# Performance work log

Hardware: AMD Instinct MI355X
Metric: run time of the kernel (lower is better)

The kernel has to match this reference:

```python
import jax, jax.numpy as jnp
import numpy as np

BS, T, LAB, DEMO, HID, F = 1024, 128, 64, 16, 32, 4


def setup_inputs() -> dict:
    key = jax.random.key(0)
    ks = jax.random.split(key, 12)
    s = 0.1
    return {
        "x": jax.random.normal(ks[0], (BS, T, LAB), dtype=jnp.float32),
        "static": jax.random.normal(ks[1], (BS, DEMO), dtype=jnp.float32),
        "demo_W": jax.random.normal(ks[2], (HID, DEMO), dtype=jnp.float32) * s,
        "demo_b": jax.random.normal(ks[3], (HID,), dtype=jnp.float32) * s,
        "lab_W": jax.random.normal(ks[4], (LAB, LAB), dtype=jnp.float32) * s,
        "lab_b": jax.random.normal(ks[5], (LAB,), dtype=jnp.float32) * s,
        # per-lab GRU weights stacked over lab_dim; input size is 1 so W_ih is [LAB, 3F]
        "Wih": jax.random.normal(ks[6], (LAB, 3 * F), dtype=jnp.float32) * 0.5,
        "bih": jax.random.normal(ks[7], (LAB, 3 * F), dtype=jnp.float32) * 0.5,
        "Whh": jax.random.normal(ks[8], (LAB, 3 * F, F), dtype=jnp.float32) * 0.5,
        "bhh": jax.random.normal(ks[9], (LAB, 3 * F), dtype=jnp.float32) * 0.5,
        "out_W": jax.random.normal(ks[10], (HID, LAB * F + HID), dtype=jnp.float32) * s,
        "out_b": jax.random.normal(ks[11], (HID,), dtype=jnp.float32) * s,
    }


def reference(x, static, demo_W, demo_b, lab_W, lab_b, Wih, bih, Whh, bhh, out_W, out_b):
    bs, t, lab = x.shape
    f = Whh.shape[-1]
    demo = static @ demo_W.T + demo_b                     # [bs, HID]
    xp = x @ lab_W.T + lab_b                              # [bs, T, LAB]

    def step(h, x_t):
        # h: [bs, LAB, F], x_t: [bs, LAB] (scalar input per lab-GRU)
        gi = x_t[:, :, None] * Wih[None] + bih[None]      # [bs, LAB, 3F]
        gh = jnp.einsum('blf,lgf->blg', h, Whh) + bhh[None]
        r = jax.nn.sigmoid(gi[..., :f] + gh[..., :f])
        z = jax.nn.sigmoid(gi[..., f:2 * f] + gh[..., f:2 * f])
        n = jnp.tanh(gi[..., 2 * f:] + r * gh[..., 2 * f:])
        h_new = (1.0 - z) * n + z * h
        return h_new, None

    h0 = jnp.zeros((bs, lab, f), dtype=x.dtype)
    h_last, _ = jax.lax.scan(step, h0, jnp.swapaxes(xp, 0, 1))  # only final step is used
    feat = h_last.reshape(bs, lab * f)                     # [bs, LAB*F]
    cat = jnp.concatenate([demo, feat], axis=-1)
    return cat @ out_W.T + out_b                           # [bs, HID]
```

## Files before the change

kernel.cpp:

```cpp
#include <hip/hip_runtime.h>
#include <cstddef>

#define BSZ   1024
#define TT    128
#define LAB   64
#define DEMO  16
#define HID   32
#define FF    4

__device__ __forceinline__ float sig_s(float p) {
    return __builtin_amdgcn_rcpf(1.0f + __builtin_amdgcn_exp2f(p));
}
__device__ __forceinline__ float tanh_s(float y) {
    return fmaf(-2.0f, __builtin_amdgcn_rcpf(__builtin_amdgcn_exp2f(y) + 1.0f), 1.0f);
}

__global__ __launch_bounds__(128)
void proj_gemm(const float* __restrict__ x,
               const float* __restrict__ lab_W,
               const float* __restrict__ lab_b,
               float* __restrict__ xp)
{
    const int b = blockIdx.x;
    const int t = threadIdx.x;

    __shared__ float wls[LAB * LAB];
    __shared__ float lbs[LAB];

    {
        const float4* src = reinterpret_cast<const float4*>(lab_W);
        float4* dst = reinterpret_cast<float4*>(wls);
        #pragma unroll
        for (int i = 0; i < 8; ++i) dst[i * 128 + t] = src[i * 128 + t];
        if (t < LAB) lbs[t] = lab_b[t];
    }

    float xr[LAB];
    const float4* xr4 = reinterpret_cast<const float4*>(x + ((size_t)b * TT + t) * LAB);
    #pragma unroll
    for (int k = 0; k < 16; ++k) {
        float4 v = xr4[k];
        xr[4*k] = v.x; xr[4*k+1] = v.y; xr[4*k+2] = v.z; xr[4*k+3] = v.w;
    }
    __syncthreads();

    float* xpb = xp + (size_t)b * LAB * TT;
    #pragma unroll 2
    for (int l = 0; l < LAB; ++l) {
        const float4* w4 = reinterpret_cast<const float4*>(wls + l * LAB);
        float a0 = 0.f, a1 = 0.f, a2 = 0.f, a3 = 0.f;
        #pragma unroll
        for (int k = 0; k < 16; ++k) {
            float4 w = w4[k];
            a0 = fmaf(w.x, xr[4*k + 0], a0);
            a1 = fmaf(w.y, xr[4*k + 1], a1);
            a2 = fmaf(w.z, xr[4*k + 2], a2);
            a3 = fmaf(w.w, xr[4*k + 3], a3);
        }
        xpb[l * TT + t] = lbs[l] + ((a0 + a1) + (a2 + a3));
    }
}

__global__ __launch_bounds__(64, 1)
void gru_kernel(const float* __restrict__ xp,
                const float* __restrict__ stat,
                const float* __restrict__ demo_W,
                const float* __restrict__ demo_b,
                const float* __restrict__ Wih,
                const float* __restrict__ bih,
                const float* __restrict__ Whh,
                const float* __restrict__ bhh,
                const float* __restrict__ out_W,
                const float* __restrict__ out_b,
                float* __restrict__ out)
{
    const int b = blockIdx.x;
    const int l = threadIdx.x;

    __shared__ float cat[HID + LAB * FF];

    const float S1 = -1.442695041f;
    const float S2 =  2.885390082f;

    float whh[48];
    #pragma unroll
    for (int k = 0; k < 48; k += 4) {
        float4 v = *reinterpret_cast<const float4*>(Whh + l * 48 + k);
        whh[k] = v.x; whh[k+1] = v.y; whh[k+2] = v.z; whh[k+3] = v.w;
    }
    float wih[12], bihv[12], bhhv[12];
    #pragma unroll
    for (int k = 0; k < 12; k += 4) {
        float4 a = *reinterpret_cast<const float4*>(Wih + l * 12 + k);
        float4 c = *reinterpret_cast<const float4*>(bih + l * 12 + k);
        float4 d = *reinterpret_cast<const float4*>(bhh + l * 12 + k);
        wih[k] = a.x; wih[k+1] = a.y; wih[k+2] = a.z; wih[k+3] = a.w;
        bihv[k] = c.x; bihv[k+1] = c.y; bihv[k+2] = c.z; bihv[k+3] = c.w;
        bhhv[k] = d.x; bhhv[k+1] = d.y; bhhv[k+2] = d.z; bhhv[k+3] = d.w;
    }
    float bc[8];
    #pragma unroll
    for (int g = 0; g < 8; ++g) {
        bc[g]  = S1 * (bihv[g] + bhhv[g]);
        wih[g] *= S1;
        #pragma unroll
        for (int k = 0; k < 4; ++k) whh[g*4 + k] *= S1;
    }
    #pragma unroll
    for (int g = 8; g < 12; ++g) {
        wih[g]  *= S2;
        bihv[g] *= S2;
        bhhv[g] *= S2;
        #pragma unroll
        for (int k = 0; k < 4; ++k) whh[g*4 + k] *= S2;
    }

    float h0 = 0.f, h1 = 0.f, h2 = 0.f, h3 = 0.f;

    const float4* xq = reinterpret_cast<const float4*>(xp + ((size_t)b * LAB + l) * TT);
    float4 xcur = xq[0];

    #pragma unroll 1
    for (int tb = 0; tb < TT / 4; ++tb) {
        float4 xnxt;
        if (tb + 1 < TT / 4) xnxt = xq[tb + 1];

        float xts[4] = {xcur.x, xcur.y, xcur.z, xcur.w};
        #pragma unroll
        for (int j = 0; j < 4; ++j) {
            const float xt = xts[j];

            float pre[8];
            #pragma unroll
            for (int g = 0; g < 8; ++g) {
                float acc = fmaf(xt, wih[g], bc[g]);
                acc = fmaf(h0, whh[g*4 + 0], acc);
                acc = fmaf(h1, whh[g*4 + 1], acc);
                acc = fmaf(h2, whh[g*4 + 2], acc);
                acc = fmaf(h3, whh[g*4 + 3], acc);
                pre[g] = acc;
            }
            const float r0 = sig_s(pre[0]);
            const float r1 = sig_s(pre[1]);
            const float r2 = sig_s(pre[2]);
            const float r3 = sig_s(pre[3]);
            const float z0 = sig_s(pre[4]);
            const float z1 = sig_s(pre[5]);
            const float z2 = sig_s(pre[6]);
            const float z3 = sig_s(pre[7]);

            float ghn[4], gin[4];
            #pragma unroll
            for (int i = 0; i < 4; ++i) {
                const int g = 8 + i;
                float acc = bhhv[g];
                acc = fmaf(h0, whh[g*4 + 0], acc);
                acc = fmaf(h1, whh[g*4 + 1], acc);
                acc = fmaf(h2, whh[g*4 + 2], acc);
                acc = fmaf(h3, whh[g*4 + 3], acc);
                ghn[i] = acc;
                gin[i] = fmaf(xt, wih[g], bihv[g]);
            }
            const float n0 = tanh_s(fmaf(r0, ghn[0], gin[0]));
            const float n1 = tanh_s(fmaf(r1, ghn[1], gin[1]));
            const float n2 = tanh_s(fmaf(r2, ghn[2], gin[2]));
            const float n3 = tanh_s(fmaf(r3, ghn[3], gin[3]));

            h0 = fmaf(z0, h0 - n0, n0);
            h1 = fmaf(z1, h1 - n1, n1);
            h2 = fmaf(z2, h2 - n2, n2);
            h3 = fmaf(z3, h3 - n3, n3);
        }
        xcur = xnxt;
    }

    cat[HID + l*4 + 0] = h0;
    cat[HID + l*4 + 1] = h1;
    cat[HID + l*4 + 2] = h2;
    cat[HID + l*4 + 3] = h3;
    if (l < HID) {
        float acc = demo_b[l];
        const float* sr = stat + (size_t)b * DEMO;
        const float* dwr = demo_W + l * DEMO;
        #pragma unroll
        for (int d = 0; d < DEMO; ++d)
            acc = fmaf(sr[d], dwr[d], acc);
        cat[l] = acc;
    }
    __syncthreads();

    if (l < HID) {
        float acc = out_b[l];
        const float* wrow = out_W + l * (HID + LAB * FF);
        #pragma unroll
        for (int i = 0; i < HID + LAB * FF; i += 4) {
            float4 wv = *reinterpret_cast<const float4*>(wrow + i);
            acc = fmaf(cat[i + 0], wv.x, acc);
            acc = fmaf(cat[i + 1], wv.y, acc);
            acc = fmaf(cat[i + 2], wv.z, acc);
            acc = fmaf(cat[i + 3], wv.w, acc);
        }
        out[(size_t)b * HID + l] = acc;
    }
}

extern "C" void kernel_launch(void* const* d_in, const int* in_sizes, int n_in,
                              void* d_out, int out_size, void* d_ws, size_t ws_size,
                              hipStream_t stream) {
    const float* x      = (const float*)d_in[0];
    const float* stat   = (const float*)d_in[1];
    const float* demo_W = (const float*)d_in[2];
    const float* demo_b = (const float*)d_in[3];
    const float* lab_W  = (const float*)d_in[4];
    const float* lab_b  = (const float*)d_in[5];
    const float* Wih    = (const float*)d_in[6];
    const float* bih    = (const float*)d_in[7];
    const float* Whh    = (const float*)d_in[8];
    const float* bhh    = (const float*)d_in[9];
    const float* out_W  = (const float*)d_in[10];
    const float* out_b  = (const float*)d_in[11];
    float* out = (float*)d_out;

    float* xp = (float*)d_ws;

    hipLaunchKernelGGL(proj_gemm, dim3(BSZ), dim3(128), 0, stream,
                       x, lab_W, lab_b, xp);
    hipLaunchKernelGGL(gru_kernel, dim3(BSZ), dim3(LAB), 0, stream,
                       xp, stat, demo_W, demo_b, Wih, bih, Whh, bhh, out_W, out_b, out);
}
```

Measured before the change: 189.2 us.

## Store projected inputs time-major and read lab_W directly from global

The projection kernel now writes xp in [b, t, lab] order with float4 stores per thread, and reads lab_W through the cache instead of staging it in shared memory, which also removes the barrier. The GRU kernel reads xp with lab-contiguous coalesced scalar loads, prefetching 8 timesteps per iteration instead of 4. The aim is to cut the strided transposed stores in the projection and the shared-memory staging cost. The trade is more registers for prefetch, and uniform weight loads that now depend on the cache.

```diff
diff --git a/kernel.cpp b/kernel.cpp
--- a/kernel.cpp
+++ b/kernel.cpp
@@ -24,17 +24,6 @@
     const int b = blockIdx.x;
     const int t = threadIdx.x;
 
-    __shared__ float wls[LAB * LAB];
-    __shared__ float lbs[LAB];
-
-    {
-        const float4* src = reinterpret_cast<const float4*>(lab_W);
-        float4* dst = reinterpret_cast<float4*>(wls);
-        #pragma unroll
-        for (int i = 0; i < 8; ++i) dst[i * 128 + t] = src[i * 128 + t];
-        if (t < LAB) lbs[t] = lab_b[t];
-    }
-
     float xr[LAB];
     const float4* xr4 = reinterpret_cast<const float4*>(x + ((size_t)b * TT + t) * LAB);
     #pragma unroll
@@ -42,22 +31,27 @@
         float4 v = xr4[k];
         xr[4*k] = v.x; xr[4*k+1] = v.y; xr[4*k+2] = v.z; xr[4*k+3] = v.w;
     }
-    __syncthreads();
-
-    float* xpb = xp + (size_t)b * LAB * TT;
+
+    float* xpb = xp + ((size_t)b * TT + t) * LAB;
     #pragma unroll 2
-    for (int l = 0; l < LAB; ++l) {
-        const float4* w4 = reinterpret_cast<const float4*>(wls + l * LAB);
-        float a0 = 0.f, a1 = 0.f, a2 = 0.f, a3 = 0.f;
-        #pragma unroll
-        for (int k = 0; k < 16; ++k) {
-            float4 w = w4[k];
-            a0 = fmaf(w.x, xr[4*k + 0], a0);
-            a1 = fmaf(w.y, xr[4*k + 1], a1);
-            a2 = fmaf(w.z, xr[4*k + 2], a2);
-            a3 = fmaf(w.w, xr[4*k + 3], a3);
-        }
-        xpb[l * TT + t] = lbs[l] + ((a0 + a1) + (a2 + a3));
+    for (int l = 0; l < LAB; l += 4) {
+        float4 o;
+        float* op = reinterpret_cast<float*>(&o);
+        #pragma unroll
+        for (int q = 0; q < 4; ++q) {
+            const float4* w4 = reinterpret_cast<const float4*>(lab_W + (l + q) * LAB);
+            float a0 = 0.f, a1 = 0.f, a2 = 0.f, a3 = 0.f;
+            #pragma unroll
+            for (int k = 0; k < 16; ++k) {
+                float4 w = w4[k];
+                a0 = fmaf(w.x, xr[4*k + 0], a0);
+                a1 = fmaf(w.y, xr[4*k + 1], a1);
+                a2 = fmaf(w.z, xr[4*k + 2], a2);
+                a3 = fmaf(w.w, xr[4*k + 3], a3);
+            }
+            op[q] = lab_b[l + q] + ((a0 + a1) + (a2 + a3));
+        }
+        *reinterpret_cast<float4*>(xpb + l) = o;
     }
 }
 
@@ -117,18 +111,22 @@
 
     float h0 = 0.f, h1 = 0.f, h2 = 0.f, h3 = 0.f;
 
-    const float4* xq = reinterpret_cast<const float4*>(xp + ((size_t)b * LAB + l) * TT);
-    float4 xcur = xq[0];
+    const float* xq = xp + (size_t)b * TT * LAB + l;
+    float cur[8], nxt[8];
+    #pragma unroll
+    for (int j = 0; j < 8; ++j) cur[j] = xq[(size_t)j * LAB];
 
     #pragma unroll 1
-    for (int tb = 0; tb < TT / 4; ++tb) {
-        float4 xnxt;
-        if (tb + 1 < TT / 4) xnxt = xq[tb + 1];
-
-        float xts[4] = {xcur.x, xcur.y, xcur.z, xcur.w};
-        #pragma unroll
-        for (int j = 0; j < 4; ++j) {
-            const float xt = xts[j];
+    for (int tb = 0; tb < TT / 8; ++tb) {
+        if (tb + 1 < TT / 8) {
+            #pragma unroll
+            for (int j = 0; j < 8; ++j)
+                nxt[j] = xq[(size_t)((tb + 1) * 8 + j) * LAB];
+        }
+
+        #pragma unroll
+        for (int j = 0; j < 8; ++j) {
+            const float xt = cur[j];
 
             float pre[8];
             #pragma unroll
@@ -171,7 +169,9 @@
             h2 = fmaf(z2, h2 - n2, n2);
             h3 = fmaf(z3, h3 - n3, n3);
         }
-        xcur = xnxt;
+
+        #pragma unroll
+        for (int j = 0; j < 8; ++j) cur[j] = nxt[j];
     }
 
     cat[HID + l*4 + 0] = h0;
```

Result: slower. 216.1 us (+14.2%).
